# Kernel optimization log

Measured on AMD Instinct MI355X. Metric: run time of the kernel, lower is better.

The kernel has to match this reference:

```python
import jax, jax.numpy as jnp
import numpy as np

N = 100000
E = 1200000
D = 64
EPS = 1e-15
ATANH_CLIP = 1.0 - 1e-7


def _logmap0(x, c):
    # Poincare ball logmap at origin: artanh(sqrt(c)||x||) * x / (sqrt(c)||x||)
    sqrt_c = jnp.sqrt(c)
    norm = jnp.maximum(jnp.linalg.norm(x, axis=-1, keepdims=True), EPS)
    arg = jnp.minimum(sqrt_c * norm, ATANH_CLIP)
    return jnp.arctanh(arg) * x / (sqrt_c * norm)


def _expmap0(u, c):
    # Poincare ball expmap at origin: tanh(sqrt(c)||u||) * u / (sqrt(c)||u||)
    sqrt_c = jnp.sqrt(c)
    norm = jnp.maximum(jnp.linalg.norm(u, axis=-1, keepdims=True), EPS)
    return jnp.tanh(sqrt_c * norm) * u / (sqrt_c * norm)


def setup_inputs() -> dict:
    key = jax.random.key(0)
    ks = jax.random.split(key, 8)
    src = jax.random.randint(ks[0], (E,), 0, N)
    dst = jax.random.randint(ks[1], (E,), 0, N)
    # scale embeddings so points lie inside the unit Poincare ball
    emb = jax.random.normal(ks[2], (N, D), dtype=jnp.float32) * 0.01
    W1 = jax.random.normal(ks[3], (D, D), dtype=jnp.float32) * 0.05
    b1 = jax.random.normal(ks[4], (D,), dtype=jnp.float32) * 0.01
    W2 = jax.random.normal(ks[5], (D, D), dtype=jnp.float32) * 0.05
    b2 = jax.random.normal(ks[6], (D,), dtype=jnp.float32) * 0.01
    curvature = -jnp.ones((1,), dtype=jnp.float32)
    return {"src": src, "dst": dst, "emb": emb, "W1": W1, "b1": b1,
            "W2": W2, "b2": b2, "curvature": curvature}


def reference(src, dst, emb, W1, b1, W2, b2, curvature):
    c = jnp.abs(curvature)[0]
    # in-degree for DGL-style mean (zero-degree nodes get 0)
    deg = jax.ops.segment_sum(jnp.ones((E,), dtype=emb.dtype), dst, num_segments=N)
    inv_deg = jnp.where(deg > 0, 1.0 / jnp.maximum(deg, 1.0), 0.0)[:, None]

    x = emb
    for W, b in ((W1, b1), (W2, b2)):
        tangent = _logmap0(x, c)                         # [N, D]
        h = tangent @ W.T + b                            # [N, D]
        neigh = jax.ops.segment_sum(h[src], dst, num_segments=N) * inv_deg  # scatter-mean
        x = _expmap0(neigh, c)
    return x
```

## Files before the change

kernel.cpp:

```cpp
#include <hip/hip_runtime.h>
#include <math.h>

#define DIM 64
#define EPSF 1e-15f

#define BW_SHIFT 9
#define BW (1 << BW_SHIFT)
#define CAP_SHIFT 13
#define CAP (1 << CAP_SHIFT)

typedef __attribute__((ext_vector_type(8))) short short8;
typedef __attribute__((ext_vector_type(4))) float floatx4;
typedef __attribute__((ext_vector_type(2))) float floatx2;
typedef __attribute__((ext_vector_type(4))) unsigned int uintx4;

__device__ __forceinline__ float group16_sum(float x) {
#pragma unroll
    for (int off = 1; off <= 8; off <<= 1)
        x += __shfl_xor(x, off, 64);
    return x;
}
__device__ __forceinline__ float group8_sum(float x) {
#pragma unroll
    for (int off = 1; off <= 4; off <<= 1)
        x += __shfl_xor(x, off, 64);
    return x;
}
__device__ __forceinline__ unsigned int f2bf(float x) {
    unsigned int u = __float_as_uint(x);
    u += 0x7fffu + ((u >> 16) & 1u);
    return u >> 16;
}
__device__ __forceinline__ float bflo(unsigned int u) { return __uint_as_float(u << 16); }
__device__ __forceinline__ float bfhi(unsigned int u) { return __uint_as_float(u & 0xFFFF0000u); }

__global__ void prep_kernel(const float* __restrict__ W1, const float* __restrict__ W2,
                            unsigned short* __restrict__ Wbf1, unsigned short* __restrict__ Wbf2,
                            unsigned short* __restrict__ zrowb, int* __restrict__ cursorB, int NB) {
    int i = blockIdx.x * 256 + threadIdx.x;
    if (i < DIM * DIM) {
        Wbf1[i] = (unsigned short)f2bf(W1[i]);
        Wbf2[i] = (unsigned short)f2bf(W2[i]);
    }
    if (i < NB) cursorB[i] = i << CAP_SHIFT;
    if (blockIdx.x == 0 && threadIdx.x < 64) zrowb[threadIdx.x] = 0;
}

__global__ __launch_bounds__(256) void partition_kernel(
    const int* __restrict__ src, const int* __restrict__ dst,
    int* __restrict__ cursorB, unsigned int* __restrict__ pairBuf, int E, int NB)
{
    __shared__ int hist[512], gbase[512], lcur[512];
    int tid = threadIdx.x;
    for (int t = tid; t < NB; t += 256) { hist[t] = 0; lcur[t] = 0; }
    __syncthreads();
    int base = blockIdx.x * 4096;
    unsigned int packed[16]; int bkt[16];
#pragma unroll
    for (int i = 0; i < 16; ++i) {
        int e = base + i * 256 + tid;
        if (e < E) {
            int s = src[e], d = dst[e];
            bkt[i] = d >> BW_SHIFT;
            packed[i] = ((unsigned int)(d & (BW - 1)) << 17) | (unsigned int)s;
            atomicAdd(&hist[bkt[i]], 1);
        } else bkt[i] = -1;
    }
    __syncthreads();
    for (int t = tid; t < NB; t += 256)
        gbase[t] = hist[t] ? atomicAdd(&cursorB[t], hist[t]) : 0;
    __syncthreads();
#pragma unroll
    for (int i = 0; i < 16; ++i) {
        if (bkt[i] >= 0) {
            int rank = atomicAdd(&lcur[bkt[i]], 1);
            int p = gbase[bkt[i]] + rank;
            if (p < ((bkt[i] + 1) << CAP_SHIFT)) pairBuf[p] = packed[i];
        }
    }
}

__global__ __launch_bounds__(512) void bucket_sort_kernel(
    const unsigned int* __restrict__ pairBuf, const int* __restrict__ cursorB,
    int* __restrict__ rowS, int* __restrict__ rowE, int* __restrict__ col, int N)
{
    __shared__ int edges[CAP];
    __shared__ int stage[CAP];
    __shared__ int hist[BW], cur[BW], tmp[BW];
    const int b = blockIdx.x, t = threadIdx.x;
    const int base = b << CAP_SHIFT;
    int cnt = cursorB[b] - base;
    if (cnt > CAP) cnt = CAP;

    for (int i = t; i < cnt; i += 512) edges[i] = (int)pairBuf[base + i];
    hist[t] = 0;
    __syncthreads();
    for (int i = t; i < cnt; i += 512) atomicAdd(&hist[edges[i] >> 17], 1);
    __syncthreads();
    int hv = hist[t];
    tmp[t] = hv; __syncthreads();
    for (int off = 1; off < 512; off <<= 1) {
        int x = (t >= off) ? tmp[t - off] : 0; __syncthreads();
        tmp[t] += x; __syncthreads();
    }
    int excl = tmp[t] - hv;
    int node = (b << BW_SHIFT) + t;
    if (node < N) { rowS[node] = base + excl; rowE[node] = base + excl + hv; }
    cur[t] = excl;
    __syncthreads();
    for (int i = t; i < cnt; i += 512) {
        int v = edges[i];
        int pos = atomicAdd(&cur[v >> 17], 1);
        stage[pos] = v & 0x1FFFF;
    }
    __syncthreads();
    for (int i = t; i < cnt; i += 512) col[base + i] = stage[i];
}

__device__ __forceinline__ void gather_rows_bf16(
    const char* __restrict__ hb, const int* __restrict__ col,
    int start, int end, int dmax, long long zoff, int g, int r, int colMax,
    floatx2 acc2[4])
{
    const int roff = r << 4;
    for (int b = 0; (b << 3) < dmax; ++b) {
        int pos = start + (b << 3) + r;
        int cv = col[min(pos, colMax)];
        int sent = (pos < end) ? cv : -1;
        int lim = dmax - (b << 3); if (lim > 8) lim = 8;
        if (lim == 8) {
            long long o[8];
#pragma unroll
            for (int i = 0; i < 8; ++i) {
                int s = __shfl(sent, (g << 3) + i, 64);
                o[i] = (s < 0) ? zoff : ((long long)s << 7);
            }
#pragma unroll
            for (int i = 0; i < 8; ++i) {
                uint4 u = *(const uint4*)(hb + o[i] + roff);
                acc2[0] += (floatx2){bflo(u.x), bfhi(u.x)};
                acc2[1] += (floatx2){bflo(u.y), bfhi(u.y)};
                acc2[2] += (floatx2){bflo(u.z), bfhi(u.z)};
                acc2[3] += (floatx2){bflo(u.w), bfhi(u.w)};
            }
        } else {
            for (int i = 0; i < lim; ++i) {
                int s = __shfl(sent, (g << 3) + i, 64);
                long long o = (s < 0) ? zoff : ((long long)s << 7);
                uint4 u = *(const uint4*)(hb + o + roff);
                acc2[0] += (floatx2){bflo(u.x), bfhi(u.x)};
                acc2[1] += (floatx2){bflo(u.y), bfhi(u.y)};
                acc2[2] += (floatx2){bflo(u.z), bfhi(u.z)};
                acc2[3] += (floatx2){bflo(u.w), bfhi(u.w)};
            }
        }
    }
}

__global__ __launch_bounds__(256, 4) void node_gemm_mfma(
    const float* __restrict__ in, const unsigned short* __restrict__ Wbf,
    const float* __restrict__ bias, const float* __restrict__ curv,
    unsigned short* __restrict__ outb, int N)
{
    __shared__ unsigned int AtileU[4][16 * 36];
    const float sc = sqrtf(fabsf(curv[0]));
    const float CLIPF = 1.0f - 1e-7f;
    const int lane = threadIdx.x & 63;
    const int wid  = threadIdx.x >> 6;
    const int q = lane >> 4, r = lane & 15;
    const int wavesTotal = (gridDim.x * blockDim.x) >> 6;
    const int numBatches = (N + 15) >> 4;
    const float4* in4 = (const float4*)in;

    short8 bfrag[4][2];
#pragma unroll
    for (int nt = 0; nt < 4; ++nt)
#pragma unroll
        for (int ks = 0; ks < 2; ++ks)
            bfrag[nt][ks] = *(const short8*)(Wbf + (nt * 16 + r) * 64 + ks * 32 + q * 8);

    float biasv[4];
#pragma unroll
    for (int nt = 0; nt < 4; ++nt) biasv[nt] = bias[nt * 16 + r];

    for (int batch = (blockIdx.x << 2) + wid; batch < numBatches; batch += wavesTotal) {
        const int base = batch << 4;
#pragma unroll
        for (int it = 0; it < 4; ++it) {
            int m = it * 4 + q;
            int node = base + m;
            float4 v = make_float4(0.f, 0.f, 0.f, 0.f);
            if (node < N) v = in4[(size_t)node * 16 + r];
            float ss = group16_sum(v.x * v.x + v.y * v.y + v.z * v.z + v.w * v.w);
            float nrm = fmaxf(sqrtf(ss), EPSF);
            float a = fminf(sc * nrm, CLIPF);
            float g = atanhf(a) / (sc * nrm);
            unsigned int lo = f2bf(v.x * g) | (f2bf(v.y * g) << 16);
            unsigned int hi = f2bf(v.z * g) | (f2bf(v.w * g) << 16);
            *(uint2*)&AtileU[wid][m * 36 + r * 2] = make_uint2(lo, hi);
        }
        floatx4 accm[4];
#pragma unroll
        for (int nt = 0; nt < 4; ++nt) accm[nt] = (floatx4){0.f, 0.f, 0.f, 0.f};
#pragma unroll
        for (int ks = 0; ks < 2; ++ks) {
            uintx4 ua = *(const uintx4*)&AtileU[wid][r * 36 + q * 4 + ks * 16];
            short8 af = __builtin_bit_cast(short8, ua);
#pragma unroll
            for (int nt = 0; nt < 4; ++nt)
                accm[nt] = __builtin_amdgcn_mfma_f32_16x16x32_bf16(af, bfrag[nt][ks], accm[nt], 0, 0, 0);
        }
#pragma unroll
        for (int nt = 0; nt < 4; ++nt)
#pragma unroll
            for (int reg = 0; reg < 4; ++reg) {
                int node = base + q * 4 + reg;
                if (node < N)
                    outb[(size_t)node * 64 + nt * 16 + r] =
                        (unsigned short)f2bf(accm[nt][reg] + biasv[nt]);
            }
    }
}

__global__ __launch_bounds__(256, 3) void gather_gemm_mfma(
    const unsigned short* __restrict__ h, const int* __restrict__ rowS,
    const int* __restrict__ rowE, const int* __restrict__ col,
    const unsigned short* __restrict__ Wbf, const float* __restrict__ bias,
    unsigned short* __restrict__ outb, long long zoff, int N, int colMax)
{
    __shared__ unsigned int AtileU[4][16 * 36];
    const int lane = threadIdx.x & 63;
    const int wid  = threadIdx.x >> 6;
    const int q = lane >> 4, r = lane & 15;
    const int g8 = lane >> 3, r8 = lane & 7;
    const int wavesTotal = (gridDim.x * blockDim.x) >> 6;
    const int numBatches = (N + 15) >> 4;
    const char* hb = (const char*)h;

    short8 bfrag[4][2];
#pragma unroll
    for (int nt = 0; nt < 4; ++nt)
#pragma unroll
        for (int ks = 0; ks < 2; ++ks)
            bfrag[nt][ks] = *(const short8*)(Wbf + (nt * 16 + r) * 64 + ks * 32 + q * 8);

    float biasv[4];
#pragma unroll
    for (int nt = 0; nt < 4; ++nt) biasv[nt] = bias[nt * 16 + r];

    for (int batch = (blockIdx.x << 2) + wid; batch < numBatches; batch += wavesTotal) {
        const int base = batch << 4;
#pragma unroll
        for (int it = 0; it < 2; ++it) {
            int m = it * 8 + g8;
            int node = base + m;
            int start = 0, end = 0;
            if (node < N) { start = rowS[node]; end = rowE[node]; }
            int deg = end - start;
            int dmax = max(deg, __shfl_xor(deg, 8, 64));
            dmax = max(dmax, __shfl_xor(dmax, 16, 64));
            dmax = max(dmax, __shfl_xor(dmax, 32, 64));
            floatx2 acc2[4] = {{0.f,0.f},{0.f,0.f},{0.f,0.f},{0.f,0.f}};
            gather_rows_bf16(hb, col, start, end, dmax, zoff, g8, r8, colMax, acc2);
            float inv = (deg > 0) ? 1.f / (float)deg : 0.f;
            unsigned int u0 = f2bf(acc2[0].x * inv) | (f2bf(acc2[0].y * inv) << 16);
            unsigned int u1 = f2bf(acc2[1].x * inv) | (f2bf(acc2[1].y * inv) << 16);
            unsigned int u2 = f2bf(acc2[2].x * inv) | (f2bf(acc2[2].y * inv) << 16);
            unsigned int u3 = f2bf(acc2[3].x * inv) | (f2bf(acc2[3].y * inv) << 16);
            *(uint4*)&AtileU[wid][m * 36 + r8 * 4] = make_uint4(u0, u1, u2, u3);
        }
        floatx4 accm[4];
#pragma unroll
        for (int nt = 0; nt < 4; ++nt) accm[nt] = (floatx4){0.f, 0.f, 0.f, 0.f};
#pragma unroll
        for (int ks = 0; ks < 2; ++ks) {
            uintx4 ua = *(const uintx4*)&AtileU[wid][r * 36 + q * 4 + ks * 16];
            short8 af = __builtin_bit_cast(short8, ua);
#pragma unroll
            for (int nt = 0; nt < 4; ++nt)
                accm[nt] = __builtin_amdgcn_mfma_f32_16x16x32_bf16(af, bfrag[nt][ks], accm[nt], 0, 0, 0);
        }
#pragma unroll
        for (int nt = 0; nt < 4; ++nt)
#pragma unroll
            for (int reg = 0; reg < 4; ++reg) {
                int node = base + q * 4 + reg;
                if (node < N)
                    outb[(size_t)node * 64 + nt * 16 + r] =
                        (unsigned short)f2bf(accm[nt][reg] + biasv[nt]);
            }
    }
}

__global__ __launch_bounds__(256, 3) void gather_expmap8(
    const unsigned short* __restrict__ h, const int* __restrict__ rowS,
    const int* __restrict__ rowE, const int* __restrict__ col,
    const float* __restrict__ curv, float* __restrict__ out,
    long long zoff, int N, int colMax)
{
    const float sc = sqrtf(fabsf(curv[0]));
    const int lane = threadIdx.x & 63;
    const int wid  = threadIdx.x >> 6;
    const int g8 = lane >> 3, r8 = lane & 7;
    const int wavesTotal = (gridDim.x * blockDim.x) >> 6;
    const int numBatches = (N + 7) >> 3;
    const char* hb = (const char*)h;
    float4* out4 = (float4*)out;

    for (int batch = (blockIdx.x << 2) + wid; batch < numBatches; batch += wavesTotal) {
        int node = (batch << 3) + g8;
        int start = 0, end = 0;
        if (node < N) { start = rowS[node]; end = rowE[node]; }
        int deg = end - start;
        int dmax = max(deg, __shfl_xor(deg, 8, 64));
        dmax = max(dmax, __shfl_xor(dmax, 16, 64));
        dmax = max(dmax, __shfl_xor(dmax, 32, 64));
        floatx2 acc2[4] = {{0.f,0.f},{0.f,0.f},{0.f,0.f},{0.f,0.f}};
        gather_rows_bf16(hb, col, start, end, dmax, zoff, g8, r8, colMax, acc2);
        float inv = (deg > 0) ? 1.f / (float)deg : 0.f;
        float v[8], ss = 0.f;
#pragma unroll
        for (int j = 0; j < 4; ++j) {
            v[2*j]   = acc2[j].x * inv;
            v[2*j+1] = acc2[j].y * inv;
            ss += v[2*j] * v[2*j] + v[2*j+1] * v[2*j+1];
        }
        ss = group8_sum(ss);
        float nrm = fmaxf(sqrtf(ss), EPSF);
        float a = sc * nrm;
        float f = tanhf(a) / a;
        if (node < N) {
            out4[(size_t)node * 16 + r8 * 2]     = make_float4(v[0] * f, v[1] * f, v[2] * f, v[3] * f);
            out4[(size_t)node * 16 + r8 * 2 + 1] = make_float4(v[4] * f, v[5] * f, v[6] * f, v[7] * f);
        }
    }
}

extern "C" void kernel_launch(void* const* d_in, const int* in_sizes, int n_in,
                              void* d_out, int out_size, void* d_ws, size_t ws_size,
                              hipStream_t stream)
{
    const int*   src  = (const int*)d_in[0];
    const int*   dst  = (const int*)d_in[1];
    const float* emb  = (const float*)d_in[2];
    const float* W1   = (const float*)d_in[3];
    const float* b1   = (const float*)d_in[4];
    const float* W2   = (const float*)d_in[5];
    const float* b2   = (const float*)d_in[6];
    const float* curv = (const float*)d_in[7];
    float*       out  = (float*)d_out;

    const int E = in_sizes[0];
    const int N = in_sizes[2] / DIM;
    const int NB = (N + BW - 1) >> BW_SHIFT;
    const size_t bucketSlots = (size_t)NB << CAP_SHIFT;
    const int colMax = (int)bucketSlots - 1;

    char* ws = (char*)d_ws;
    auto align256 = [](size_t x) { return (x + 255) & ~(size_t)255; };
    size_t off = 0;
    int* cursorB            = (int*)(ws + off);            off += align256(512 * 4);
    int* rowS               = (int*)(ws + off);            off += align256((size_t)N * 4);
    int* rowE               = (int*)(ws + off);            off += align256((size_t)N * 4);
    unsigned int* pairBuf   = (unsigned int*)(ws + off);   off += align256(bucketSlots * 4);
    int* col                = (int*)(ws + off);            off += align256(bucketSlots * 4);
    unsigned short* Wbf1    = (unsigned short*)(ws + off); off += align256((size_t)DIM * DIM * 2);
    unsigned short* Wbf2    = (unsigned short*)(ws + off); off += align256((size_t)DIM * DIM * 2);
    unsigned short* zrowb   = (unsigned short*)(ws + off); off += align256(DIM * 2);
    unsigned short* h1b     = (unsigned short*)(ws + off); off += align256((size_t)N * DIM * 2);
    unsigned short* h2b     = (unsigned short*)(ws + off); off += align256((size_t)N * DIM * 2);

    const long long zoff_h1 = (long long)((char*)zrowb - (char*)h1b);
    const long long zoff_h2 = (long long)((char*)zrowb - (char*)h2b);

    const int chunkBlocks  = (E + 4095) / 4096;
    const int numBatches16 = (N + 15) / 16;
    const int blocks16     = (numBatches16 + 3) / 4;
    const int numBatches8  = (N + 7) / 8;
    const int blocks8      = (numBatches8 + 3) / 4;

    prep_kernel<<<(DIM * DIM + 255) / 256, 256, 0, stream>>>(W1, W2, Wbf1, Wbf2,
                                                             zrowb, cursorB, NB);
    partition_kernel<<<chunkBlocks, 256, 0, stream>>>(src, dst, cursorB, pairBuf, E, NB);
    bucket_sort_kernel<<<NB, 512, 0, stream>>>(pairBuf, cursorB, rowS, rowE, col, N);

    node_gemm_mfma<<<blocks16, 256, 0, stream>>>(emb, Wbf1, b1, curv, h1b, N);
    gather_gemm_mfma<<<blocks16, 256, 0, stream>>>(h1b, rowS, rowE, col, Wbf2, b2, h2b,
                                                   zoff_h1, N, colMax);
    gather_expmap8<<<blocks8, 256, 0, stream>>>(h2b, rowS, rowE, col, curv, out,
                                                zoff_h2, N, colMax);
}
```

Before: 193.8 us.

## Merge bucket sort and first-layer node GEMM into one concurrent launch

```diff
diff --git a/kernel.cpp b/kernel.cpp
--- a/kernel.cpp
+++ b/kernel.cpp
@@ -4,9 +4,9 @@
 #define DIM 64
 #define EPSF 1e-15f
 
-#define BW_SHIFT 9
+#define BW_SHIFT 8
 #define BW (1 << BW_SHIFT)
-#define CAP_SHIFT 13
+#define CAP_SHIFT 12
 #define CAP (1 << CAP_SHIFT)
 
 typedef __attribute__((ext_vector_type(8))) short short8;
@@ -80,41 +80,111 @@
     }
 }
 
-__global__ __launch_bounds__(512) void bucket_sort_kernel(
+union SharedU {
+    struct {
+        int edges[CAP];
+        int stage[CAP];
+        int hist[BW], cur[BW], tmp[BW];
+    } s;
+    unsigned int atile[4][16 * 36];
+};
+
+__global__ __launch_bounds__(256, 4) void sort_and_gemm_kernel(
     const unsigned int* __restrict__ pairBuf, const int* __restrict__ cursorB,
-    int* __restrict__ rowS, int* __restrict__ rowE, int* __restrict__ col, int N)
-{
-    __shared__ int edges[CAP];
-    __shared__ int stage[CAP];
-    __shared__ int hist[BW], cur[BW], tmp[BW];
-    const int b = blockIdx.x, t = threadIdx.x;
-    const int base = b << CAP_SHIFT;
-    int cnt = cursorB[b] - base;
-    if (cnt > CAP) cnt = CAP;
-
-    for (int i = t; i < cnt; i += 512) edges[i] = (int)pairBuf[base + i];
-    hist[t] = 0;
-    __syncthreads();
-    for (int i = t; i < cnt; i += 512) atomicAdd(&hist[edges[i] >> 17], 1);
-    __syncthreads();
-    int hv = hist[t];
-    tmp[t] = hv; __syncthreads();
-    for (int off = 1; off < 512; off <<= 1) {
-        int x = (t >= off) ? tmp[t - off] : 0; __syncthreads();
-        tmp[t] += x; __syncthreads();
-    }
-    int excl = tmp[t] - hv;
-    int node = (b << BW_SHIFT) + t;
-    if (node < N) { rowS[node] = base + excl; rowE[node] = base + excl + hv; }
-    cur[t] = excl;
-    __syncthreads();
-    for (int i = t; i < cnt; i += 512) {
-        int v = edges[i];
-        int pos = atomicAdd(&cur[v >> 17], 1);
-        stage[pos] = v & 0x1FFFF;
-    }
-    __syncthreads();
-    for (int i = t; i < cnt; i += 512) col[base + i] = stage[i];
+    int* __restrict__ rowS, int* __restrict__ rowE, int* __restrict__ col,
+    const float* __restrict__ in, const unsigned short* __restrict__ Wbf,
+    const float* __restrict__ bias, const float* __restrict__ curv,
+    unsigned short* __restrict__ outb, int N, int NB)
+{
+    __shared__ SharedU u;
+    if ((int)blockIdx.x < NB) {
+        const int b = blockIdx.x, t = threadIdx.x;
+        const int base = b << CAP_SHIFT;
+        int cnt = cursorB[b] - base;
+        if (cnt > CAP) cnt = CAP;
+        for (int i = t; i < cnt; i += 256) u.s.edges[i] = (int)pairBuf[base + i];
+        u.s.hist[t] = 0;
+        __syncthreads();
+        for (int i = t; i < cnt; i += 256) atomicAdd(&u.s.hist[u.s.edges[i] >> 17], 1);
+        __syncthreads();
+        int hv = u.s.hist[t];
+        u.s.tmp[t] = hv; __syncthreads();
+        for (int off = 1; off < 256; off <<= 1) {
+            int x = (t >= off) ? u.s.tmp[t - off] : 0; __syncthreads();
+            u.s.tmp[t] += x; __syncthreads();
+        }
+        int excl = u.s.tmp[t] - hv;
+        int node = (b << BW_SHIFT) + t;
+        if (node < N) { rowS[node] = base + excl; rowE[node] = base + excl + hv; }
+        u.s.cur[t] = excl;
+        __syncthreads();
+        for (int i = t; i < cnt; i += 256) {
+            int v = u.s.edges[i];
+            int pos = atomicAdd(&u.s.cur[v >> 17], 1);
+            u.s.stage[pos] = v & 0x1FFFF;
+        }
+        __syncthreads();
+        for (int i = t; i < cnt; i += 256) col[base + i] = u.s.stage[i];
+    } else {
+        const int bid = blockIdx.x - NB;
+        const int gemmWaves = (gridDim.x - NB) << 2;
+        const float sc = sqrtf(fabsf(curv[0]));
+        const float CLIPF = 1.0f - 1e-7f;
+        const int lane = threadIdx.x & 63;
+        const int wid  = threadIdx.x >> 6;
+        const int q = lane >> 4, r = lane & 15;
+        const int numBatches = (N + 15) >> 4;
+        const float4* in4 = (const float4*)in;
+
+        short8 bfrag[4][2];
+#pragma unroll
+        for (int nt = 0; nt < 4; ++nt)
+#pragma unroll
+            for (int ks = 0; ks < 2; ++ks)
+                bfrag[nt][ks] = *(const short8*)(Wbf + (nt * 16 + r) * 64 + ks * 32 + q * 8);
+
+        float biasv[4];
+#pragma unroll
+        for (int nt = 0; nt < 4; ++nt) biasv[nt] = bias[nt * 16 + r];
+
+        for (int batch = (bid << 2) + wid; batch < numBatches; batch += gemmWaves) {
+            const int base = batch << 4;
+#pragma unroll
+            for (int it = 0; it < 4; ++it) {
+                int m = it * 4 + q;
+                int node = base + m;
+                float4 v = make_float4(0.f, 0.f, 0.f, 0.f);
+                if (node < N) v = in4[(size_t)node * 16 + r];
+                float ss = group16_sum(v.x * v.x + v.y * v.y + v.z * v.z + v.w * v.w);
+                float nrm = fmaxf(sqrtf(ss), EPSF);
+                float a = fminf(sc * nrm, CLIPF);
+                float g = atanhf(a) / (sc * nrm);
+                unsigned int lo = f2bf(v.x * g) | (f2bf(v.y * g) << 16);
+                unsigned int hi = f2bf(v.z * g) | (f2bf(v.w * g) << 16);
+                *(uint2*)&u.atile[wid][m * 36 + r * 2] = make_uint2(lo, hi);
+            }
+            floatx4 accm[4];
+#pragma unroll
+            for (int nt = 0; nt < 4; ++nt) accm[nt] = (floatx4){0.f, 0.f, 0.f, 0.f};
+#pragma unroll
+            for (int ks = 0; ks < 2; ++ks) {
+                uintx4 ua = *(const uintx4*)&u.atile[wid][r * 36 + q * 4 + ks * 16];
+                short8 af = __builtin_bit_cast(short8, ua);
+#pragma unroll
+                for (int nt = 0; nt < 4; ++nt)
+                    accm[nt] = __builtin_amdgcn_mfma_f32_16x16x32_bf16(af, bfrag[nt][ks], accm[nt], 0, 0, 0);
+            }
+#pragma unroll
+            for (int nt = 0; nt < 4; ++nt)
+#pragma unroll
+                for (int reg = 0; reg < 4; ++reg) {
+                    int node = base + q * 4 + reg;
+                    if (node < N)
+                        outb[(size_t)node * 64 + nt * 16 + r] =
+                            (unsigned short)f2bf(accm[nt][reg] + biasv[nt]);
+                }
+        }
+    }
 }
 
 __device__ __forceinline__ void gather_rows_bf16(
@@ -137,92 +207,27 @@
             }
 #pragma unroll
             for (int i = 0; i < 8; ++i) {
-                uint4 u = *(const uint4*)(hb + o[i] + roff);
-                acc2[0] += (floatx2){bflo(u.x), bfhi(u.x)};
-                acc2[1] += (floatx2){bflo(u.y), bfhi(u.y)};
-                acc2[2] += (floatx2){bflo(u.z), bfhi(u.z)};
-                acc2[3] += (floatx2){bflo(u.w), bfhi(u.w)};
+                uint4 uu = *(const uint4*)(hb + o[i] + roff);
+                acc2[0] += (floatx2){bflo(uu.x), bfhi(uu.x)};
+                acc2[1] += (floatx2){bflo(uu.y), bfhi(uu.y)};
+                acc2[2] += (floatx2){bflo(uu.z), bfhi(uu.z)};
+                acc2[3] += (floatx2){bflo(uu.w), bfhi(uu.w)};
             }
         } else {
             for (int i = 0; i < lim; ++i) {
                 int s = __shfl(sent, (g << 3) + i, 64);
                 long long o = (s < 0) ? zoff : ((long long)s << 7);
-                uint4 u = *(const uint4*)(hb + o + roff);
-                acc2[0] += (floatx2){bflo(u.x), bfhi(u.x)};
-                acc2[1] += (floatx2){bflo(u.y), bfhi(u.y)};
-                acc2[2] += (floatx2){bflo(u.z), bfhi(u.z)};
-                acc2[3] += (floatx2){bflo(u.w), bfhi(u.w)};
-            }
-        }
-    }
-}
-
-__global__ __launch_bounds__(256, 4) void node_gemm_mfma(
-    const float* __restrict__ in, const unsigned short* __restrict__ Wbf,
-    const float* __restrict__ bias, const float* __restrict__ curv,
-    unsigned short* __restrict__ outb, int N)
-{
-    __shared__ unsigned int AtileU[4][16 * 36];
-    const float sc = sqrtf(fabsf(curv[0]));
-    const float CLIPF = 1.0f - 1e-7f;
-    const int lane = threadIdx.x & 63;
-    const int wid  = threadIdx.x >> 6;
-    const int q = lane >> 4, r = lane & 15;
-    const int wavesTotal = (gridDim.x * blockDim.x) >> 6;
-    const int numBatches = (N + 15) >> 4;
-    const float4* in4 = (const float4*)in;
-
-    short8 bfrag[4][2];
-#pragma unroll
-    for (int nt = 0; nt < 4; ++nt)
-#pragma unroll
-        for (int ks = 0; ks < 2; ++ks)
-            bfrag[nt][ks] = *(const short8*)(Wbf + (nt * 16 + r) * 64 + ks * 32 + q * 8);
-
-    float biasv[4];
-#pragma unroll
-    for (int nt = 0; nt < 4; ++nt) biasv[nt] = bias[nt * 16 + r];
-
-    for (int batch = (blockIdx.x << 2) + wid; batch < numBatches; batch += wavesTotal) {
-        const int base = batch << 4;
-#pragma unroll
-        for (int it = 0; it < 4; ++it) {
-            int m = it * 4 + q;
-            int node = base + m;
-            float4 v = make_float4(0.f, 0.f, 0.f, 0.f);
-            if (node < N) v = in4[(size_t)node * 16 + r];
-            float ss = group16_sum(v.x * v.x + v.y * v.y + v.z * v.z + v.w * v.w);
-            float nrm = fmaxf(sqrtf(ss), EPSF);
-            float a = fminf(sc * nrm, CLIPF);
-            float g = atanhf(a) / (sc * nrm);
-            unsigned int lo = f2bf(v.x * g) | (f2bf(v.y * g) << 16);
-            unsigned int hi = f2bf(v.z * g) | (f2bf(v.w * g) << 16);
-            *(uint2*)&AtileU[wid][m * 36 + r * 2] = make_uint2(lo, hi);
-        }
-        floatx4 accm[4];
-#pragma unroll
-        for (int nt = 0; nt < 4; ++nt) accm[nt] = (floatx4){0.f, 0.f, 0.f, 0.f};
-#pragma unroll
-        for (int ks = 0; ks < 2; ++ks) {
-            uintx4 ua = *(const uintx4*)&AtileU[wid][r * 36 + q * 4 + ks * 16];
-            short8 af = __builtin_bit_cast(short8, ua);
-#pragma unroll
-            for (int nt = 0; nt < 4; ++nt)
-                accm[nt] = __builtin_amdgcn_mfma_f32_16x16x32_bf16(af, bfrag[nt][ks], accm[nt], 0, 0, 0);
-        }
-#pragma unroll
-        for (int nt = 0; nt < 4; ++nt)
-#pragma unroll
-            for (int reg = 0; reg < 4; ++reg) {
-                int node = base + q * 4 + reg;
-                if (node < N)
-                    outb[(size_t)node * 64 + nt * 16 + r] =
-                        (unsigned short)f2bf(accm[nt][reg] + biasv[nt]);
-            }
-    }
-}
-
-__global__ __launch_bounds__(256, 3) void gather_gemm_mfma(
+                uint4 uu = *(const uint4*)(hb + o + roff);
+                acc2[0] += (floatx2){bflo(uu.x), bfhi(uu.x)};
+                acc2[1] += (floatx2){bflo(uu.y), bfhi(uu.y)};
+                acc2[2] += (floatx2){bflo(uu.z), bfhi(uu.z)};
+                acc2[3] += (floatx2){bflo(uu.w), bfhi(uu.w)};
+            }
+        }
+    }
+}
+
+__global__ __launch_bounds__(256, 4) void gather_gemm_mfma(
     const unsigned short* __restrict__ h, const int* __restrict__ rowS,
     const int* __restrict__ rowE, const int* __restrict__ col,
     const unsigned short* __restrict__ Wbf, const float* __restrict__ bias,
@@ -292,7 +297,7 @@
     }
 }
 
-__global__ __launch_bounds__(256, 3) void gather_expmap8(
+__global__ __launch_bounds__(256, 6) void gather_expmap8(
     const unsigned short* __restrict__ h, const int* __restrict__ rowS,
     const int* __restrict__ rowE, const int* __restrict__ col,
     const float* __restrict__ curv, float* __restrict__ out,
@@ -382,9 +387,8 @@
     prep_kernel<<<(DIM * DIM + 255) / 256, 256, 0, stream>>>(W1, W2, Wbf1, Wbf2,
                                                              zrowb, cursorB, NB);
     partition_kernel<<<chunkBlocks, 256, 0, stream>>>(src, dst, cursorB, pairBuf, E, NB);
-    bucket_sort_kernel<<<NB, 512, 0, stream>>>(pairBuf, cursorB, rowS, rowE, col, N);
-
-    node_gemm_mfma<<<blocks16, 256, 0, stream>>>(emb, Wbf1, b1, curv, h1b, N);
+    sort_and_gemm_kernel<<<NB + blocks16, 256, 0, stream>>>(
+        pairBuf, cursorB, rowS, rowE, col, emb, Wbf1, b1, curv, h1b, N, NB);
     gather_gemm_mfma<<<blocks16, 256, 0, stream>>>(h1b, rowS, rowE, col, Wbf2, b2, h2b,
                                                    zoff_h1, N, colMax);
     gather_expmap8<<<blocks8, 256, 0, stream>>>(h2b, rowS, rowE, col, curv, out,
```

Measured after the change: 188.3 us. -2.9%, faster.
